# Performance work log

Measured on AMD Instinct MI355X. Metric: run time of the kernel, lower is better.

## Reference

```python
import jax, jax.numpy as jnp
import numpy as np

V, E, H, TAGS = 50000, 128, 128, 8  # H = hidden per direction (hidden_dim // 2)
B, T = 64, 512


def _lstm_dir(x, w_ih, w_hh, b_ih, b_hh, reverse):
    # x: [B,T,I] -> hs: [B,T,H]; PyTorch gate order i,f,g,o
    xg = jnp.einsum('bti,gi->btg', x, w_ih) + b_ih + b_hh  # [B,T,4H]
    if reverse:
        xg = xg[:, ::-1]
    Bn = x.shape[0]
    Hn = w_hh.shape[1]

    def step(carry, g):
        h, c = carry
        g = g + h @ w_hh.T
        i, f, gg, o = jnp.split(g, 4, axis=-1)
        c = jax.nn.sigmoid(f) * c + jax.nn.sigmoid(i) * jnp.tanh(gg)
        h = jax.nn.sigmoid(o) * jnp.tanh(c)
        return (h, c), h

    h0 = jnp.zeros((Bn, Hn), x.dtype)
    _, hs = jax.lax.scan(step, (h0, h0), jnp.swapaxes(xg, 0, 1))
    hs = jnp.swapaxes(hs, 0, 1)
    return hs[:, ::-1] if reverse else hs


def _crf_partition(emissions, transitions):
    # emissions: [B,T,K]; scan the forward algorithm over time
    fv0 = emissions[:, 0]  # [B,K]

    def step(fv, emit):
        fv = jax.nn.logsumexp(fv[:, :, None] + transitions[None] + emit[:, None, :], axis=1)
        return fv, None

    fv, _ = jax.lax.scan(step, fv0, jnp.swapaxes(emissions[:, 1:], 0, 1))
    return jax.nn.logsumexp(fv, axis=1)  # [B]


def _forward_nll(sentences, tags, embedding, lstm_params, h2t_w, h2t_b, transitions):
    x = embedding[sentences]  # [B,T,E]; dropout inactive (eval)
    for pf, pb in lstm_params:
        x = jnp.concatenate([_lstm_dir(x, *pf, False), _lstm_dir(x, *pb, True)], axis=-1)
    emissions = x @ h2t_w.T + h2t_b  # [B,T,K]
    # gold path score (mask = all ones)
    emit_score = jnp.take_along_axis(emissions, tags[:, :, None], axis=2)[..., 0].sum(axis=1)
    trans_score = transitions[tags[:, :-1], tags[:, 1:]].sum(axis=1)
    partition = _crf_partition(emissions, transitions)
    return -(emit_score + trans_score - partition).mean()


def setup_inputs() -> dict:
    key = jax.random.key(0)
    ks = jax.random.split(key, 40)
    sc = 0.05
    inp = {}
    inp['sentences'] = jax.random.randint(ks[0], (B, T), 0, V)
    inp['tags'] = jax.random.randint(ks[1], (B, T), 0, TAGS)
    emb = jax.random.normal(ks[2], (V, E), jnp.float32) * sc
    inp['embedding'] = emb.at[0].set(0.0)  # padding_idx=0
    idx = 3
    for l in range(2):
        in_dim = E if l == 0 else 2 * H
        for d in ('', '_rev'):
            inp[f'w_ih_l{l}{d}'] = jax.random.normal(ks[idx], (4 * H, in_dim), jnp.float32) * sc; idx += 1
            inp[f'w_hh_l{l}{d}'] = jax.random.normal(ks[idx], (4 * H, H), jnp.float32) * sc; idx += 1
            inp[f'b_ih_l{l}{d}'] = jax.random.normal(ks[idx], (4 * H,), jnp.float32) * sc; idx += 1
            inp[f'b_hh_l{l}{d}'] = jax.random.normal(ks[idx], (4 * H,), jnp.float32) * sc; idx += 1
    inp['h2t_w'] = jax.random.normal(ks[idx], (TAGS, 2 * H), jnp.float32) * sc; idx += 1
    inp['h2t_b'] = jax.random.normal(ks[idx], (TAGS,), jnp.float32) * sc; idx += 1
    trans = jax.random.normal(ks[idx], (TAGS, TAGS), jnp.float32)
    inp['transitions'] = trans.at[0, :].set(-10000.0).at[:, 0].set(-10000.0)
    return inp


def reference(sentences, tags, embedding,
              w_ih_l0, w_hh_l0, b_ih_l0, b_hh_l0,
              w_ih_l0_rev, w_hh_l0_rev, b_ih_l0_rev, b_hh_l0_rev,
              w_ih_l1, w_hh_l1, b_ih_l1, b_hh_l1,
              w_ih_l1_rev, w_hh_l1_rev, b_ih_l1_rev, b_hh_l1_rev,
              h2t_w, h2t_b, transitions):
    lstm_params = [
        ((w_ih_l0, w_hh_l0, b_ih_l0, b_hh_l0), (w_ih_l0_rev, w_hh_l0_rev, b_ih_l0_rev, b_hh_l0_rev)),
        ((w_ih_l1, w_hh_l1, b_ih_l1, b_hh_l1), (w_ih_l1_rev, w_hh_l1_rev, b_ih_l1_rev, b_hh_l1_rev)),
    ]
    return _forward_nll(sentences, tags, embedding, lstm_params, h2t_w, h2t_b, transitions)
```

## Files before the change

### kernel.cpp

```cpp
#include <hip/hip_runtime.h>
#include <cstdint>
#include <cstddef>

typedef __attribute__((ext_vector_type(8))) short bf16x8;
typedef __attribute__((ext_vector_type(8))) int   v8i;
typedef __attribute__((ext_vector_type(4))) float f32x4;

__device__ __forceinline__ unsigned short f2bf(float x) {
    union { float f; unsigned u; } v; v.f = x;
    unsigned r = (v.u + 0x7fffu + ((v.u >> 16) & 1u)) >> 16;
    return (unsigned short)r;
}
__device__ __forceinline__ unsigned short f2bf_trunc(float x) {
    union { float f; unsigned u; } v; v.f = x;
    return (unsigned short)(v.u >> 16);
}
__device__ __forceinline__ float bflo(unsigned u){ union{unsigned i;float f;}v; v.i = u << 16;        return v.f; }
__device__ __forceinline__ float bfhi(unsigned u){ union{unsigned i;float f;}v; v.i = u & 0xffff0000u; return v.f; }
__device__ __forceinline__ float frcp(float x){ return __builtin_amdgcn_rcpf(x); }
__device__ __forceinline__ float ex2(float x){ return __builtin_amdgcn_exp2f(x); }

#define BARRIER_LGKM() asm volatile("s_waitcnt lgkmcnt(0)\n\ts_barrier" ::: "memory")

#define BB 64
#define TT 512
#define MM (BB*TT)
#define NG 1024

#define NL2E  -1.442695f
#define N2L2E -2.885390f

__device__ __forceinline__ int perm_orig(int g2) {
    return (g2 & 3) * 128 + (g2 >> 6) * 16 + ((g2 >> 4) & 3) * 4 + ((g2 >> 2) & 3);
}

__global__ void prep_kernel(
    const int* __restrict__ sentences, const float* __restrict__ emb,
    const float* __restrict__ w_ih_l0, const float* __restrict__ w_ih_l0r,
    const float* __restrict__ w_ih_l1, const float* __restrict__ w_ih_l1r,
    const float* __restrict__ w_hh_l0, const float* __restrict__ w_hh_l0r,
    const float* __restrict__ w_hh_l1, const float* __restrict__ w_hh_l1r,
    const float* __restrict__ b_ih_l0, const float* __restrict__ b_hh_l0,
    const float* __restrict__ b_ih_l0r, const float* __restrict__ b_hh_l0r,
    const float* __restrict__ b_ih_l1, const float* __restrict__ b_hh_l1,
    const float* __restrict__ b_ih_l1r, const float* __restrict__ b_hh_l1r,
    unsigned short* __restrict__ x0, unsigned short* __restrict__ W0c,
    unsigned short* __restrict__ W1c,
    int* __restrict__ Whh0q, int* __restrict__ Whh1q,
    float* __restrict__ bias0, float* __restrict__ bias1)
{
    int blk = blockIdx.x;
    if (blk < 4096) {
        int t4 = blk * 256 + threadIdx.x;
        int e4 = t4 * 4; int m = e4 >> 7; int k = e4 & 127;
        int tt = m >> 6, b = m & 63;
        int s = sentences[b * 512 + tt];
        float4 v = *(const float4*)(emb + (size_t)s * 128 + k);
        *(ushort4*)(x0 + (size_t)m * 128 + k) =
            make_ushort4(f2bf(v.x), f2bf(v.y), f2bf(v.z), f2bf(v.w));
    } else if (blk < 4224) {
        int t4 = (blk - 4096) * 256 + threadIdx.x;
        int e4 = t4 * 4; int n = e4 >> 7; int k = e4 & 127;
        int dir = n >> 9; int orig = perm_orig(n & 511);
        const float* src = dir ? w_ih_l0r : w_ih_l0;
        float4 v = *(const float4*)(src + (size_t)orig * 128 + k);
        *(ushort4*)(W0c + (size_t)n * 128 + k) =
            make_ushort4(f2bf(v.x), f2bf(v.y), f2bf(v.z), f2bf(v.w));
    } else if (blk < 4480) {
        int t4 = (blk - 4224) * 256 + threadIdx.x;
        int e4 = t4 * 4; int n = e4 >> 8; int k = e4 & 255;
        int dir = n >> 9; int orig = perm_orig(n & 511);
        const float* src = dir ? w_ih_l1r : w_ih_l1;
        float4 v = *(const float4*)(src + (size_t)orig * 256 + k);
        *(ushort4*)(W1c + (size_t)n * 256 + k) =
            make_ushort4(f2bf(v.x), f2bf(v.y), f2bf(v.z), f2bf(v.w));
    } else if (blk < 4736) {
        int lb = blk - 4480;
        int layer = lb >> 7;
        int t4 = (lb & 127) * 256 + threadIdx.x;
        int f  = t4 * 4;
        int j0   = f & 31;
        int lp   = (f >> 5) & 63;
        int quad = lp >> 4, r = lp & 15;
        int tb   = f >> 11;
        int tile = tb & 3, w = (tb >> 2) & 7, dir = tb >> 5;
        int g2 = w * 64 + tile * 16 + r;
        int orig = perm_orig(g2);
        const float* src = layer ? (dir ? w_hh_l1r : w_hh_l1)
                                 : (dir ? w_hh_l0r : w_hh_l0);
        int k = quad * 32 + j0;
        float fac = ((r & 3) == 2) ? (N2L2E * 64.f) : (NL2E * 64.f);
        float4 v = *(const float4*)(src + (size_t)orig * 128 + k);
        int p = __builtin_amdgcn_cvt_pk_fp8_f32(v.x * fac, v.y * fac, 0, false);
        p = __builtin_amdgcn_cvt_pk_fp8_f32(v.z * fac, v.w * fac, p, true);
        (layer ? Whh1q : Whh0q)[f >> 2] = p;
    } else {
        int t = (blk - 4736) * 256 + threadIdx.x;
        int n = t & 1023;
        int dir = n >> 9; int orig = perm_orig(n & 511);
        if (t < 1024)
            bias0[n] = dir ? (b_ih_l0r[orig] + b_hh_l0r[orig]) : (b_ih_l0[orig] + b_hh_l0[orig]);
        else
            bias1[n] = dir ? (b_ih_l1r[orig] + b_hh_l1r[orig]) : (b_ih_l1[orig] + b_hh_l1[orig]);
    }
}

__global__ __launch_bounds__(256, 2) void gemm_xg(
    const unsigned short* __restrict__ W,
    const unsigned short* __restrict__ X,
    const float* __restrict__ bias,
    unsigned short* __restrict__ xgS,
    int K)
{
    __shared__ unsigned short sW[128 * 32];
    __shared__ unsigned short sX[128 * 32];
    const int tid  = threadIdx.x;
    const int lane = tid & 63;
    const int wid  = tid >> 6;
    const int w_n  = wid & 1, w_m = wid >> 1;
    const int r16  = lane & 15, quad = lane >> 4;
    const int nTile = blockIdx.x * 128;
    const int mTile = blockIdx.y * 128;

    f32x4 zero = {0.f, 0.f, 0.f, 0.f};
    f32x4 acc[4][4];
    #pragma unroll
    for (int i = 0; i < 4; ++i)
        #pragma unroll
        for (int j = 0; j < 4; ++j) acc[i][j] = zero;

    const int q0 = tid, q1 = tid + 256;
    const int r0 = q0 >> 2, c0 = q0 & 3, ko0 = c0 * 8;
    const int r1 = q1 >> 2, c1 = q1 & 3, ko1 = c1 * 8;
    const int s0 = (r0 << 2) | (c0 ^ ((r0 >> 1) & 3));
    const int s1 = (r1 << 2) | (c1 ^ ((r1 >> 1) & 3));
    const int rsw = quad ^ ((r16 >> 1) & 3);

    const unsigned short* Wp0 = W + (size_t)(nTile + r0) * K + ko0;
    const unsigned short* Wp1 = W + (size_t)(nTile + r1) * K + ko1;
    const unsigned short* Xp0 = X + (size_t)(mTile + r0) * K + ko0;
    const unsigned short* Xp1 = X + (size_t)(mTile + r1) * K + ko1;

    uint4 wv0 = *(const uint4*)(Wp0);
    uint4 wv1 = *(const uint4*)(Wp1);
    uint4 xv0 = *(const uint4*)(Xp0);
    uint4 xv1 = *(const uint4*)(Xp1);

    for (int k0 = 0; k0 < K; k0 += 32) {
        BARRIER_LGKM();
        ((uint4*)sW)[s0] = wv0;
        ((uint4*)sW)[s1] = wv1;
        ((uint4*)sX)[s0] = xv0;
        ((uint4*)sX)[s1] = xv1;
        BARRIER_LGKM();
        if (k0 + 32 < K) {
            wv0 = *(const uint4*)(Wp0 + k0 + 32);
            wv1 = *(const uint4*)(Wp1 + k0 + 32);
            xv0 = *(const uint4*)(Xp0 + k0 + 32);
            xv1 = *(const uint4*)(Xp1 + k0 + 32);
        }
        const bf16x8* sWv = (const bf16x8*)sW;
        const bf16x8* sXv = (const bf16x8*)sX;
        bf16x8 a[4], bx[4];
        #pragma unroll
        for (int i = 0; i < 4; ++i) {
            a[i]  = sWv[((w_n * 64 + i * 16 + r16) << 2) | rsw];
            bx[i] = sXv[((w_m * 64 + i * 16 + r16) << 2) | rsw];
        }
        #pragma unroll
        for (int i = 0; i < 4; ++i)
            #pragma unroll
            for (int j = 0; j < 4; ++j)
                acc[i][j] = __builtin_amdgcn_mfma_f32_16x16x32_bf16(a[i], bx[j], acc[i][j], 0, 0, 0);
    }

    const int w_idx = ((nTile & 511) >> 6) + w_n;
    const int dirn  = nTile >> 9;
    float4 bv[4];
    #pragma unroll
    for (int i = 0; i < 4; ++i)
        bv[i] = *(const float4*)(bias + nTile + w_n * 64 + i * 16 + quad * 4);
    const int t  = (mTile >> 6) + w_m;
    const size_t pbase = (size_t)(t >> 1) * 131072 + (size_t)dirn * 65536
                       + (size_t)w_idx * 512 + (size_t)(t & 1) * 4;
    #pragma unroll
    for (int j = 0; j < 4; ++j) {
        int b = j * 16 + r16;
        size_t base = pbase + (size_t)(b >> 2) * 4096;
        #pragma unroll
        for (int i = 0; i < 4; ++i) {
            f32x4 v = acc[i][j];
            ushort4 o = make_ushort4(f2bf((v.x + bv[i].x) * NL2E),
                                     f2bf((v.y + bv[i].y) * NL2E),
                                     f2bf((v.z + bv[i].z) * N2L2E),
                                     f2bf((v.w + bv[i].w) * NL2E));
            *(uint2*)(xgS + base + (size_t)(quad * 16 + i * 4 + (b & 3)) * 8) = *(uint2*)&o;
        }
    }
}

__global__ __launch_bounds__(512, 1) void lstm_scan_mfma(
    const unsigned short* __restrict__ xgS,
    const unsigned char* __restrict__ whh_q,
    unsigned short* __restrict__ xnext)
{
    const int dir = blockIdx.x >> 4;
    const int bg  = blockIdx.x & 15;
    const int tid = threadIdx.x;
    const int w   = tid >> 6;
    const int lane= tid & 63;
    const int q   = lane >> 4;
    const int bl  = lane & 15;
    const int d   = bl >> 2;
    const int b4  = bl & 3;
    const int u   = w * 16 + d * 4 + q;
    const int b   = bg * 4 + b4;

    v8i afrag[4];
    {
        const unsigned char* wb = whh_q + (size_t)dir * 65536 + (size_t)w * 8192 + lane * 32;
        #pragma unroll
        for (int tile = 0; tile < 4; ++tile) {
            uint4 a0 = *(const uint4*)(wb + tile * 2048);
            uint4 a1 = *(const uint4*)(wb + tile * 2048 + 16);
            v8i av; av[0]=a0.x; av[1]=a0.y; av[2]=a0.z; av[3]=a0.w;
                    av[4]=a1.x; av[5]=a1.y; av[6]=a1.z; av[7]=a1.w;
            afrag[tile] = av;
        }
    }

    __shared__ __align__(16) unsigned char hbuf[2][576];
    if (tid < 144) ((unsigned*)hbuf[1])[tid] = 0;

    float c = 0.f;
    const long pstep = dir ? -131072L : 131072L;
    const unsigned short* xp = xgS + (size_t)(dir ? 255 : 0) * 131072
                             + (size_t)dir * 65536 + bg * 4096 + w * 512 + lane * 8;
    const long hstep = dir ? -16384L : 16384L;
    long hoff = (long)(dir ? 511 : 0) * 16384 + (long)b * 256 + dir * 128 + u;

    const int hw  = b4 * 144 + u;
    const int hr  = b4 * 144 + q * 32;

    auto step_body = [&](uint2 xv, const unsigned char* rb, unsigned char* wbuf) {
        uint4 h0 = *(const uint4*)(rb + hr);
        uint4 h1 = *(const uint4*)(rb + hr + 16);
        v8i bfr; bfr[0]=h0.x; bfr[1]=h0.y; bfr[2]=h0.z; bfr[3]=h0.w;
                 bfr[4]=h1.x; bfr[5]=h1.y; bfr[6]=h1.z; bfr[7]=h1.w;
        f32x4 gv;
        gv.x = bflo(xv.x); gv.y = bfhi(xv.x);
        gv.z = bflo(xv.y); gv.w = bfhi(xv.y);
        f32x4 a0 = gv, a1 = gv, a2 = gv, a3 = gv;
        a0 = __builtin_amdgcn_mfma_scale_f32_16x16x128_f8f6f4(afrag[0], bfr, a0, 0, 0,
                 0, 0x79797979, 0, 0x7B7B7B7B);
        a1 = __builtin_amdgcn_mfma_scale_f32_16x16x128_f8f6f4(afrag[1], bfr, a1, 0, 0,
                 0, 0x79797979, 0, 0x7B7B7B7B);
        a2 = __builtin_amdgcn_mfma_scale_f32_16x16x128_f8f6f4(afrag[2], bfr, a2, 0, 0,
                 0, 0x79797979, 0, 0x7B7B7B7B);
        a3 = __builtin_amdgcn_mfma_scale_f32_16x16x128_f8f6f4(afrag[3], bfr, a3, 0, 0,
                 0, 0x79797979, 0, 0x7B7B7B7B);
        f32x4 sel = a0;
        sel = (d == 1) ? a1 : sel;
        sel = (d == 2) ? a2 : sel;
        sel = (d == 3) ? a3 : sel;
        float si = frcp(1.f + ex2(sel.x));
        float sf = frcp(1.f + ex2(sel.y));
        float tg = 2.f * frcp(1.f + ex2(sel.z)) - 1.f;
        float so = frcp(1.f + ex2(sel.w));
        c = sf * c + si * tg;
        float tc = 2.f * frcp(1.f + ex2(N2L2E * c)) - 1.f;
        float h = so * tc;
        xnext[hoff] = f2bf_trunc(h);
        hoff += hstep;
        int q8 = __builtin_amdgcn_cvt_pk_fp8_f32(h * 16.f, h * 16.f, 0, false);
        wbuf[hw] = (unsigned char)(q8 & 0xff);
        BARRIER_LGKM();
    };

    uint4 ring[4];
    #pragma unroll
    for (int i = 0; i < 4; ++i)
        ring[i] = *(const uint4*)(xp + (long)i * pstep);

    BARRIER_LGKM();

    for (int it2 = 0; it2 < 64; ++it2) {
        #pragma unroll
        for (int pp = 0; pp < 4; ++pp) {
            uint4 rv = ring[pp];
            uint2 xa, xb;
            if (dir) { xa.x = rv.z; xa.y = rv.w; xb.x = rv.x; xb.y = rv.y; }
            else     { xa.x = rv.x; xa.y = rv.y; xb.x = rv.z; xb.y = rv.w; }
            ring[pp] = *(const uint4*)(xp + 4 * pstep);
            xp += pstep;
            step_body(xa, hbuf[1], hbuf[0]);
            step_body(xb, hbuf[0], hbuf[1]);
        }
    }
}

__global__ void emis_kernel(const unsigned short* __restrict__ x2,
                            const float* __restrict__ h2t_w,
                            const float* __restrict__ h2t_b,
                            float* __restrict__ emis)
{
    int idx = blockIdx.x * 256 + threadIdx.x;
    int m = idx >> 3, tag = idx & 7;
    const unsigned short* xr = x2 + (size_t)m * 256;
    const float* wr = h2t_w + (size_t)tag * 256;
    float a0 = 0.f, a1 = 0.f, a2 = 0.f, a3 = 0.f;
    #pragma unroll 4
    for (int k = 0; k < 256; k += 8) {
        uint4 xv = *(const uint4*)(xr + k);
        float4 w0 = *(const float4*)(wr + k);
        float4 w1 = *(const float4*)(wr + k + 4);
        a0 += bflo(xv.x) * w0.x + bfhi(xv.x) * w0.y;
        a1 += bflo(xv.y) * w0.z + bfhi(xv.y) * w0.w;
        a2 += bflo(xv.z) * w1.x + bfhi(xv.z) * w1.y;
        a3 += bflo(xv.w) * w1.z + bfhi(xv.w) * w1.w;
    }
    emis[idx] = h2t_b[tag] + ((a0 + a1) + (a2 + a3));
}

__global__ void crf_chunk(const float* __restrict__ emis,
                          const float* __restrict__ trans,
                          float* __restrict__ Pc)
{
    const int b = blockIdx.x >> 3;
    const int cch = blockIdx.x & 7;
    const int l = threadIdx.x;
    const int i = l >> 3, j = l & 7;
    const int i8 = i * 8;
    float T[8];
    #pragma unroll
    for (int k = 0; k < 8; ++k) T[k] = trans[k * 8 + j];

    const int t0 = (cch == 0) ? 1 : cch * 64;
    const int t1 = cch * 64 + 64;
    const float* ej = emis + (size_t)b * 8 + j;

    float P = trans[i * 8 + j] + ej[(size_t)t0 * 512];
    float e1 = ej[(size_t)(t0 + 1) * 512];
    for (int t = t0 + 1; t < t1; ++t) {
        float v0 = __shfl(P, i8 + 0) + T[0];
        float v1 = __shfl(P, i8 + 1) + T[1];
        float v2 = __shfl(P, i8 + 2) + T[2];
        float v3 = __shfl(P, i8 + 3) + T[3];
        float v4 = __shfl(P, i8 + 4) + T[4];
        float v5 = __shfl(P, i8 + 5) + T[5];
        float v6 = __shfl(P, i8 + 6) + T[6];
        float v7 = __shfl(P, i8 + 7) + T[7];
        float m = fmaxf(fmaxf(fmaxf(v0, v1), fmaxf(v2, v3)),
                        fmaxf(fmaxf(v4, v5), fmaxf(v6, v7)));
        float s = __expf(v0 - m) + __expf(v1 - m) + __expf(v2 - m) + __expf(v3 - m)
                + __expf(v4 - m) + __expf(v5 - m) + __expf(v6 - m) + __expf(v7 - m);
        P = m + __logf(s) + e1;
        e1 = ej[(size_t)(t + 1) * 512];
    }
    Pc[((size_t)b * 8 + cch) * 64 + l] = P;
}

__global__ void crf_combine(const float* __restrict__ emis,
                            const float* __restrict__ Pc,
                            const int* __restrict__ tags,
                            const float* __restrict__ trans,
                            float* __restrict__ out)
{
    const int l = threadIdx.x;
    const int sl = l >> 3, j = l & 7, sl8 = sl * 8;
    const int b = blockIdx.x * 8 + sl;

    float fv = emis[(size_t)b * 8 + j];
    #pragma unroll
    for (int cch = 0; cch < 8; ++cch) {
        const float* Pb = Pc + ((size_t)b * 8 + cch) * 64 + j;
        float p0 = Pb[0],  p1 = Pb[8],  p2 = Pb[16], p3 = Pb[24];
        float p4 = Pb[32], p5 = Pb[40], p6 = Pb[48], p7 = Pb[56];
        float v0 = __shfl(fv, sl8 + 0) + p0;
        float v1 = __shfl(fv, sl8 + 1) + p1;
        float v2 = __shfl(fv, sl8 + 2) + p2;
        float v3 = __shfl(fv, sl8 + 3) + p3;
        float v4 = __shfl(fv, sl8 + 4) + p4;
        float v5 = __shfl(fv, sl8 + 5) + p5;
        float v6 = __shfl(fv, sl8 + 6) + p6;
        float v7 = __shfl(fv, sl8 + 7) + p7;
        float m = fmaxf(fmaxf(fmaxf(v0, v1), fmaxf(v2, v3)),
                        fmaxf(fmaxf(v4, v5), fmaxf(v6, v7)));
        float s = __expf(v0 - m) + __expf(v1 - m) + __expf(v2 - m) + __expf(v3 - m)
                + __expf(v4 - m) + __expf(v5 - m) + __expf(v6 - m) + __expf(v7 - m);
        fv = m + __logf(s);
    }

    float m2 = fv;
    m2 = fmaxf(m2, __shfl_xor(m2, 1));
    m2 = fmaxf(m2, __shfl_xor(m2, 2));
    m2 = fmaxf(m2, __shfl_xor(m2, 4));
    float e2s = __expf(fv - m2);
    e2s += __shfl_xor(e2s, 1);
    e2s += __shfl_xor(e2s, 2);
    e2s += __shfl_xor(e2s, 4);
    float partition = m2 + __logf(e2s);

    const int* tg = tags + (size_t)b * TT;
    float sc = 0.f;
    for (int tt = j; tt < TT; tt += 8) {
        int tag = tg[tt];
        sc += emis[((size_t)tt * 64 + b) * 8 + tag];
        if (tt > 0) sc += trans[tg[tt - 1] * 8 + tag];
    }
    sc += __shfl_xor(sc, 1);
    sc += __shfl_xor(sc, 2);
    sc += __shfl_xor(sc, 4);

    float val = (j == 0) ? (partition - sc) * 0.015625f : 0.f;
    #pragma unroll
    for (int dd = 1; dd < 64; dd <<= 1) val += __shfl_xor(val, dd);
    if (l == 0) atomicAdd(out, val);
}

extern "C" void kernel_launch(void* const* d_in, const int* in_sizes, int n_in,
                              void* d_out, int out_size, void* d_ws, size_t ws_size,
                              hipStream_t stream)
{
    const int*   sentences = (const int*)d_in[0];
    const int*   tags      = (const int*)d_in[1];
    const float* embedding = (const float*)d_in[2];
    const float* w_ih_l0   = (const float*)d_in[3];
    const float* w_hh_l0   = (const float*)d_in[4];
    const float* b_ih_l0   = (const float*)d_in[5];
    const float* b_hh_l0   = (const float*)d_in[6];
    const float* w_ih_l0r  = (const float*)d_in[7];
    const float* w_hh_l0r  = (const float*)d_in[8];
    const float* b_ih_l0r  = (const float*)d_in[9];
    const float* b_hh_l0r  = (const float*)d_in[10];
    const float* w_ih_l1   = (const float*)d_in[11];
    const float* w_hh_l1   = (const float*)d_in[12];
    const float* b_ih_l1   = (const float*)d_in[13];
    const float* b_hh_l1   = (const float*)d_in[14];
    const float* w_ih_l1r  = (const float*)d_in[15];
    const float* w_hh_l1r  = (const float*)d_in[16];
    const float* b_ih_l1r  = (const float*)d_in[17];
    const float* b_hh_l1r  = (const float*)d_in[18];
    const float* h2t_w     = (const float*)d_in[19];
    const float* h2t_b     = (const float*)d_in[20];
    const float* trans     = (const float*)d_in[21];

    char* ws = (char*)d_ws;
    unsigned short* W0c   = (unsigned short*)(ws + 0);
    unsigned short* W1c   = (unsigned short*)(ws + 262144);
    int*  Whh0q           = (int*)(ws + 786432);
    int*  Whh1q           = (int*)(ws + 917504);
    float* bias0          = (float*)(ws + 1310720);
    float* bias1          = (float*)(ws + 1314816);
    float* emis           = (float*)(ws + 1318912);
    float* Pc             = (float*)(ws + 2375936);
    unsigned short* xgS   = (unsigned short*)(ws + 4194304);
    unsigned short* x0    = (unsigned short*)(ws + 71303168);
    unsigned short* x1    = (unsigned short*)(ws + 72351744);
    unsigned short* x2    = x1;
    (void)ws_size; (void)in_sizes; (void)n_in; (void)out_size;

    hipMemsetAsync(d_out, 0, sizeof(float), stream);

    prep_kernel<<<4744, 256, 0, stream>>>(sentences, embedding,
        w_ih_l0, w_ih_l0r, w_ih_l1, w_ih_l1r,
        w_hh_l0, w_hh_l0r, w_hh_l1, w_hh_l1r,
        b_ih_l0, b_hh_l0, b_ih_l0r, b_hh_l0r,
        b_ih_l1, b_hh_l1, b_ih_l1r, b_hh_l1r,
        x0, W0c, W1c, Whh0q, Whh1q, bias0, bias1);

    gemm_xg<<<dim3(8, 256), 256, 0, stream>>>(W0c, x0, bias0, xgS, 128);
    lstm_scan_mfma<<<32, 512, 0, stream>>>(xgS, (const unsigned char*)Whh0q, x1);
    gemm_xg<<<dim3(8, 256), 256, 0, stream>>>(W1c, x1, bias1, xgS, 256);
    lstm_scan_mfma<<<32, 512, 0, stream>>>(xgS, (const unsigned char*)Whh1q, x2);
    emis_kernel<<<1024, 256, 0, stream>>>(x2, h2t_w, h2t_b, emis);
    crf_chunk<<<512, 64, 0, stream>>>(emis, trans, Pc);
    crf_combine<<<8, 64, 0, stream>>>(emis, Pc, tags, trans, (float*)d_out);
}
```

Measured before the change: 608.9 us.

## Halve LSTM scan block to 4 waves, each handling two hidden-unit groups

The recurrent scan kernel now runs 256 threads (4 waves) per block instead of 512, and each wave owns 32 hidden units. It holds 8 fp8 weight fragments and issues 8 MFMAs per step, with two cell states per lane. The hidden-unit permutation, the W_hh packing in prep and the xg output layout in the GEMM epilogue are all rewritten to match. The aim is to shorten the per-step barrier across fewer waves and to raise work per wave on the serial critical path, at the cost of more MFMA and gate math per wave each step.

New measurement: 685.3 us. 12.5% more time.

```diff
diff --git a/kernel.cpp b/kernel.cpp
--- a/kernel.cpp
+++ b/kernel.cpp
@@ -31,7 +31,7 @@
 #define N2L2E -2.885390f
 
 __device__ __forceinline__ int perm_orig(int g2) {
-    return (g2 & 3) * 128 + (g2 >> 6) * 16 + ((g2 >> 4) & 3) * 4 + ((g2 >> 2) & 3);
+    return (g2 & 3) * 128 + (g2 >> 7) * 32 + ((g2 >> 4) & 7) * 4 + ((g2 >> 2) & 3);
 }
 
 __global__ void prep_kernel(
@@ -80,16 +80,18 @@
         int t4 = (lb & 127) * 256 + threadIdx.x;
         int f  = t4 * 4;
         int j0   = f & 31;
-        int lp   = (f >> 5) & 63;
-        int quad = lp >> 4, r = lp & 15;
-        int tb   = f >> 11;
-        int tile = tb & 3, w = (tb >> 2) & 7, dir = tb >> 5;
-        int g2 = w * 64 + tile * 16 + r;
-        int orig = perm_orig(g2);
+        int lane = (f >> 5) & 63;
+        int t8   = (f >> 11) & 7;
+        int w4   = (f >> 14) & 3;
+        int dir  = f >> 16;
+        int r16 = lane & 15, quad = lane >> 4;
+        int unit  = w4 * 32 + t8 * 4 + (r16 >> 2);
+        int gtype = r16 & 3;
+        int orig = gtype * 128 + unit;
         const float* src = layer ? (dir ? w_hh_l1r : w_hh_l1)
                                  : (dir ? w_hh_l0r : w_hh_l0);
         int k = quad * 32 + j0;
-        float fac = ((r & 3) == 2) ? (N2L2E * 64.f) : (NL2E * 64.f);
+        float fac = (gtype == 2) ? (N2L2E * 64.f) : (NL2E * 64.f);
         float4 v = *(const float4*)(src + (size_t)orig * 128 + k);
         int p = __builtin_amdgcn_cvt_pk_fp8_f32(v.x * fac, v.y * fac, 0, false);
         p = __builtin_amdgcn_cvt_pk_fp8_f32(v.z * fac, v.w * fac, p, true);
@@ -174,32 +176,33 @@
                 acc[i][j] = __builtin_amdgcn_mfma_f32_16x16x32_bf16(a[i], bx[j], acc[i][j], 0, 0, 0);
     }
 
-    const int w_idx = ((nTile & 511) >> 6) + w_n;
-    const int dirn  = nTile >> 9;
+    const int dirn = nTile >> 9;
     float4 bv[4];
     #pragma unroll
     for (int i = 0; i < 4; ++i)
         bv[i] = *(const float4*)(bias + nTile + w_n * 64 + i * 16 + quad * 4);
-    const int t  = (mTile >> 6) + w_m;
-    const size_t pbase = (size_t)(t >> 1) * 131072 + (size_t)dirn * 65536
-                       + (size_t)w_idx * 512 + (size_t)(t & 1) * 4;
+    const int t_m = (mTile >> 6) + w_m;
     #pragma unroll
     for (int j = 0; j < 4; ++j) {
         int b = j * 16 + r16;
-        size_t base = pbase + (size_t)(b >> 2) * 4096;
+        size_t bb = (size_t)t_m * 65536 + (size_t)dirn * 32768 + (size_t)(b >> 2) * 2048
+                  + (size_t)(quad * 16 + (b & 3)) * 8;
         #pragma unroll
         for (int i = 0; i < 4; ++i) {
+            int g2l = (nTile & 511) + w_n * 64 + i * 16 + quad * 4;
+            int t8 = (g2l >> 4) & 7, w4 = g2l >> 7;
             f32x4 v = acc[i][j];
             ushort4 o = make_ushort4(f2bf((v.x + bv[i].x) * NL2E),
                                      f2bf((v.y + bv[i].y) * NL2E),
                                      f2bf((v.z + bv[i].z) * N2L2E),
                                      f2bf((v.w + bv[i].w) * NL2E));
-            *(uint2*)(xgS + base + (size_t)(quad * 16 + i * 4 + (b & 3)) * 8) = *(uint2*)&o;
+            size_t off = bb + (size_t)w4 * 512 + (size_t)(t8 & 3) * 32 + (size_t)(t8 >> 2) * 4;
+            *(uint2*)(xgS + off) = *(uint2*)&o;
         }
     }
 }
 
-__global__ __launch_bounds__(512, 1) void lstm_scan_mfma(
+__global__ __launch_bounds__(256, 1) void lstm_scan_mfma(
     const unsigned short* __restrict__ xgS,
     const unsigned char* __restrict__ whh_q,
     unsigned short* __restrict__ xnext)
@@ -213,67 +216,87 @@
     const int bl  = lane & 15;
     const int d   = bl >> 2;
     const int b4  = bl & 3;
-    const int u   = w * 16 + d * 4 + q;
+    const int uA  = w * 32 + d * 4 + q;
     const int b   = bg * 4 + b4;
 
-    v8i afrag[4];
+    v8i afrag[8];
     {
-        const unsigned char* wb = whh_q + (size_t)dir * 65536 + (size_t)w * 8192 + lane * 32;
-        #pragma unroll
-        for (int tile = 0; tile < 4; ++tile) {
-            uint4 a0 = *(const uint4*)(wb + tile * 2048);
-            uint4 a1 = *(const uint4*)(wb + tile * 2048 + 16);
+        const unsigned char* wb = whh_q + (size_t)dir * 65536 + (size_t)w * 16384 + lane * 32;
+        #pragma unroll
+        for (int t = 0; t < 8; ++t) {
+            uint4 a0 = *(const uint4*)(wb + t * 2048);
+            uint4 a1 = *(const uint4*)(wb + t * 2048 + 16);
             v8i av; av[0]=a0.x; av[1]=a0.y; av[2]=a0.z; av[3]=a0.w;
                     av[4]=a1.x; av[5]=a1.y; av[6]=a1.z; av[7]=a1.w;
-            afrag[tile] = av;
+            afrag[t] = av;
         }
     }
 
     __shared__ __align__(16) unsigned char hbuf[2][576];
     if (tid < 144) ((unsigned*)hbuf[1])[tid] = 0;
 
-    float c = 0.f;
-    const long pstep = dir ? -131072L : 131072L;
-    const unsigned short* xp = xgS + (size_t)(dir ? 255 : 0) * 131072
-                             + (size_t)dir * 65536 + bg * 4096 + w * 512 + lane * 8;
+    float cA = 0.f, cB = 0.f;
+    const long pstep = dir ? -65536L : 65536L;
+    const unsigned short* xp = xgS + (size_t)(dir ? 511 : 0) * 65536
+                             + (size_t)dir * 32768 + bg * 2048 + w * 512 + lane * 8;
     const long hstep = dir ? -16384L : 16384L;
-    long hoff = (long)(dir ? 511 : 0) * 16384 + (long)b * 256 + dir * 128 + u;
-
-    const int hw  = b4 * 144 + u;
+    long hoff = (long)(dir ? 511 : 0) * 16384 + (long)b * 256 + dir * 128 + uA;
+
+    const int hwA = b4 * 144 + uA;
     const int hr  = b4 * 144 + q * 32;
 
-    auto step_body = [&](uint2 xv, const unsigned char* rb, unsigned char* wbuf) {
+    auto step_body = [&](uint4 xv, const unsigned char* rb, unsigned char* wbuf) {
         uint4 h0 = *(const uint4*)(rb + hr);
         uint4 h1 = *(const uint4*)(rb + hr + 16);
         v8i bfr; bfr[0]=h0.x; bfr[1]=h0.y; bfr[2]=h0.z; bfr[3]=h0.w;
                  bfr[4]=h1.x; bfr[5]=h1.y; bfr[6]=h1.z; bfr[7]=h1.w;
-        f32x4 gv;
-        gv.x = bflo(xv.x); gv.y = bfhi(xv.x);
-        gv.z = bflo(xv.y); gv.w = bfhi(xv.y);
-        f32x4 a0 = gv, a1 = gv, a2 = gv, a3 = gv;
-        a0 = __builtin_amdgcn_mfma_scale_f32_16x16x128_f8f6f4(afrag[0], bfr, a0, 0, 0,
-                 0, 0x79797979, 0, 0x7B7B7B7B);
-        a1 = __builtin_amdgcn_mfma_scale_f32_16x16x128_f8f6f4(afrag[1], bfr, a1, 0, 0,
-                 0, 0x79797979, 0, 0x7B7B7B7B);
-        a2 = __builtin_amdgcn_mfma_scale_f32_16x16x128_f8f6f4(afrag[2], bfr, a2, 0, 0,
-                 0, 0x79797979, 0, 0x7B7B7B7B);
-        a3 = __builtin_amdgcn_mfma_scale_f32_16x16x128_f8f6f4(afrag[3], bfr, a3, 0, 0,
-                 0, 0x79797979, 0, 0x7B7B7B7B);
-        f32x4 sel = a0;
-        sel = (d == 1) ? a1 : sel;
-        sel = (d == 2) ? a2 : sel;
-        sel = (d == 3) ? a3 : sel;
-        float si = frcp(1.f + ex2(sel.x));
-        float sf = frcp(1.f + ex2(sel.y));
-        float tg = 2.f * frcp(1.f + ex2(sel.z)) - 1.f;
-        float so = frcp(1.f + ex2(sel.w));
-        c = sf * c + si * tg;
-        float tc = 2.f * frcp(1.f + ex2(N2L2E * c)) - 1.f;
-        float h = so * tc;
-        xnext[hoff] = f2bf_trunc(h);
+        f32x4 gvA, gvB;
+        gvA.x = bflo(xv.x); gvA.y = bfhi(xv.x);
+        gvA.z = bflo(xv.y); gvA.w = bfhi(xv.y);
+        gvB.x = bflo(xv.z); gvB.y = bfhi(xv.z);
+        gvB.z = bflo(xv.w); gvB.w = bfhi(xv.w);
+        f32x4 r0 = __builtin_amdgcn_mfma_scale_f32_16x16x128_f8f6f4(afrag[0], bfr, gvA, 0, 0,
+                       0, 0x79797979, 0, 0x7B7B7B7B);
+        f32x4 r1 = __builtin_amdgcn_mfma_scale_f32_16x16x128_f8f6f4(afrag[1], bfr, gvA, 0, 0,
+                       0, 0x79797979, 0, 0x7B7B7B7B);
+        f32x4 r2 = __builtin_amdgcn_mfma_scale_f32_16x16x128_f8f6f4(afrag[2], bfr, gvA, 0, 0,
+                       0, 0x79797979, 0, 0x7B7B7B7B);
+        f32x4 r3 = __builtin_amdgcn_mfma_scale_f32_16x16x128_f8f6f4(afrag[3], bfr, gvA, 0, 0,
+                       0, 0x79797979, 0, 0x7B7B7B7B);
+        f32x4 r4 = __builtin_amdgcn_mfma_scale_f32_16x16x128_f8f6f4(afrag[4], bfr, gvB, 0, 0,
+                       0, 0x79797979, 0, 0x7B7B7B7B);
+        f32x4 r5 = __builtin_amdgcn_mfma_scale_f32_16x16x128_f8f6f4(afrag[5], bfr, gvB, 0, 0,
+                       0, 0x79797979, 0, 0x7B7B7B7B);
+        f32x4 r6 = __builtin_amdgcn_mfma_scale_f32_16x16x128_f8f6f4(afrag[6], bfr, gvB, 0, 0,
+                       0, 0x79797979, 0, 0x7B7B7B7B);
+        f32x4 r7 = __builtin_amdgcn_mfma_scale_f32_16x16x128_f8f6f4(afrag[7], bfr, gvB, 0, 0,
+                       0, 0x79797979, 0, 0x7B7B7B7B);
+        f32x4 sA = r0;
+        sA = (d == 1) ? r1 : sA;
+        sA = (d == 2) ? r2 : sA;
+        sA = (d == 3) ? r3 : sA;
+        f32x4 sB = r4;
+        sB = (d == 1) ? r5 : sB;
+        sB = (d == 2) ? r6 : sB;
+        sB = (d == 3) ? r7 : sB;
+        float siA = frcp(1.f + ex2(sA.x));
+        float sfA = frcp(1.f + ex2(sA.y));
+        float tgA = 2.f * frcp(1.f + ex2(sA.z)) - 1.f;
+        float soA = frcp(1.f + ex2(sA.w));
+        cA = sfA * cA + siA * tgA;
+        float hA = soA * (2.f * frcp(1.f + ex2(N2L2E * cA)) - 1.f);
+        float siB = frcp(1.f + ex2(sB.x));
+        float sfB = frcp(1.f + ex2(sB.y));
+        float tgB = 2.f * frcp(1.f + ex2(sB.z)) - 1.f;
+        float soB = frcp(1.f + ex2(sB.w));
+        cB = sfB * cB + siB * tgB;
+        float hB = soB * (2.f * frcp(1.f + ex2(N2L2E * cB)) - 1.f);
+        int pk = __builtin_amdgcn_cvt_pk_fp8_f32(hA * 16.f, hB * 16.f, 0, false);
+        wbuf[hwA]      = (unsigned char)(pk & 0xff);
+        wbuf[hwA + 16] = (unsigned char)((pk >> 8) & 0xff);
+        xnext[hoff]      = f2bf_trunc(hA);
+        xnext[hoff + 16] = f2bf_trunc(hB);
         hoff += hstep;
-        int q8 = __builtin_amdgcn_cvt_pk_fp8_f32(h * 16.f, h * 16.f, 0, false);
-        wbuf[hw] = (unsigned char)(q8 & 0xff);
         BARRIER_LGKM();
     };
 
@@ -284,17 +307,13 @@
 
     BARRIER_LGKM();
 
-    for (int it2 = 0; it2 < 64; ++it2) {
+    for (int it = 0; it < 128; ++it) {
         #pragma unroll
         for (int pp = 0; pp < 4; ++pp) {
-            uint4 rv = ring[pp];
-            uint2 xa, xb;
-            if (dir) { xa.x = rv.z; xa.y = rv.w; xb.x = rv.x; xb.y = rv.y; }
-            else     { xa.x = rv.x; xa.y = rv.y; xb.x = rv.z; xb.y = rv.w; }
+            uint4 xv = ring[pp];
             ring[pp] = *(const uint4*)(xp + 4 * pstep);
             xp += pstep;
-            step_body(xa, hbuf[1], hbuf[0]);
-            step_body(xb, hbuf[0], hbuf[1]);
+            step_body(xv, hbuf[(pp & 1) ^ 1], hbuf[pp & 1]);
         }
     }
 }
@@ -470,9 +489,9 @@
         x0, W0c, W1c, Whh0q, Whh1q, bias0, bias1);
 
     gemm_xg<<<dim3(8, 256), 256, 0, stream>>>(W0c, x0, bias0, xgS, 128);
-    lstm_scan_mfma<<<32, 512, 0, stream>>>(xgS, (const unsigned char*)Whh0q, x1);
+    lstm_scan_mfma<<<32, 256, 0, stream>>>(xgS, (const unsigned char*)Whh0q, x1);
     gemm_xg<<<dim3(8, 256), 256, 0, stream>>>(W1c, x1, bias1, xgS, 256);
-    lstm_scan_mfma<<<32, 512, 0, stream>>>(xgS, (const unsigned char*)Whh1q, x2);
+    lstm_scan_mfma<<<32, 256, 0, stream>>>(xgS, (const unsigned char*)Whh1q, x2);
     emis_kernel<<<1024, 256, 0, stream>>>(x2, h2t_w, h2t_b, emis);
     crf_chunk<<<512, 64, 0, stream>>>(emis, trans, Pc);
     crf_combine<<<8, 64, 0, stream>>>(emis, Pc, tags, trans, (float*)d_out);
```
